# Kernel tuning notes

Hardware: AMD Instinct MI355X
Metric: run time of the kernel (lower is better)

## Reference

```python
import jax, jax.numpy as jnp
from jax import lax
import numpy as np

RADIUS = 5
ITERATION = 10
IMG_SHAPE = (2048, 2048, 3)


def make_side_window_kernels(r):
    # 8 directional side-window box kernels, each (2r+1)x(2r+1), minus identity at center
    k = np.ones((2 * r + 1, 1), dtype=np.float64) / (2 * r + 1)
    k_L = k.copy()
    k_L[r + 1:] = 0
    k_L = k_L / np.sum(k_L)
    k_R = k_L[::-1, :]

    def get_kernel(a, b):
        # repeat(a, K, axis=1) * repeat(b.T, K, axis=0) == outer(a, b)
        ab = a @ b.T
        ab = ab.copy()
        ab[r, r] -= 1.0  # residual form: filter - identity
        return ab

    kernel = np.stack([
        get_kernel(k_L, k_L), get_kernel(k_L, k_R),
        get_kernel(k_R, k_L), get_kernel(k_R, k_R),
        get_kernel(k_L, k), get_kernel(k_R, k),
        get_kernel(k, k_L), get_kernel(k, k_R),
    ]).astype(np.float32)
    return kernel[:, np.newaxis, :, :]  # (8, 1, K, K) OIHW


def setup_inputs() -> dict:
    key = jax.random.key(0)
    img = jax.random.uniform(key, IMG_SHAPE, dtype=jnp.float32)
    kernel = jnp.asarray(make_side_window_kernels(RADIUS))
    return {"img": img, "kernel": kernel}


def reference(img, kernel):
    r = RADIUS
    # edge-pad once (numpy 'edge' == jnp 'edge')
    U0 = jnp.pad(img, ((r, r), (r, r), (0, 0)), mode="edge")  # (Hp, Wp, C)

    def step(U, _):
        x = jnp.transpose(U, (2, 0, 1))[:, None]  # (C, 1, Hp, Wp)
        # cross-correlation with zero padding r (matches torch Conv2d padding=r)
        d = lax.conv_general_dilated(x, kernel, (1, 1), [(r, r), (r, r)])  # (C, 8, Hp, Wp)
        idx = jnp.argmin(jnp.abs(d), axis=1, keepdims=True)  # (C, 1, Hp, Wp)
        dm = jnp.take_along_axis(d, idx, axis=1)[:, 0]        # (C, Hp, Wp)
        return U + jnp.transpose(dm, (1, 2, 0)), None

    U, _ = lax.scan(step, U0, None, length=ITERATION)
    return U[r:-r, r:-r, :]
```

## Files before the change

kernel.cpp:

```cpp
#include <hip/hip_runtime.h>

#define H 2048
#define W 2048
#define C 3
#define RAD 5
#define P (H + 2*RAD)
#define RS 2064
#define PLANE ((size_t)P * RS)
#define NITER 10

#define BX 64
#define BY 16
#define EX (BX + 2*RAD)
#define EY (BY + 2*RAD)
#define LSTR (EX + 1)

__global__ void pad_kernel(const float* __restrict__ img, float* __restrict__ dst, int c) {
    int idx = blockIdx.x * blockDim.x + threadIdx.x;
    int total = P * P;
    if (idx >= total) return;
    int y = idx / P;
    int x = idx - y * P;
    int ys = min(max(y - RAD, 0), H - 1);
    int xs = min(max(x - RAD, 0), W - 1);
    dst[(size_t)y * RS + x] = img[((size_t)ys * W + xs) * C + c];
}

__global__ __launch_bounds__(256)
void step_kernel(const float* __restrict__ src, float* __restrict__ dst,
                 const float* __restrict__ kern) {
    __shared__ float sU[EY][LSTR];

    const float w36 = kern[0];
    const float c36 = kern[5 * 11 + 5];
    const float w66 = kern[4 * 121];
    const float c66 = kern[4 * 121 + 5 * 11 + 5];

    const int x0 = blockIdx.x * BX;
    const int y0 = blockIdx.y * BY;
    const int tid = threadIdx.y * 64 + threadIdx.x;

    for (int i = tid; i < EY * EX; i += 256) {
        int r   = i / EX;
        int col = i - r * EX;
        int gy = y0 - RAD + r;
        int gx = x0 - RAD + col;
        float v = 0.0f;
        if (gy >= 0 && gy < P && gx >= 0 && gx < P)
            v = src[(size_t)gy * RS + gx];
        sU[r][col] = v;
    }
    __syncthreads();

    const int tx = threadIdx.x;
    const int gx = x0 + tx;
    const bool xok = (gx < P);

    #pragma unroll 1
    for (int rr = threadIdx.y; rr < BY; rr += 4) {
        int gy = y0 + rr;
        if (!xok || gy >= P) continue;

        float a0 = 0.f, a1 = 0.f, a2 = 0.f, a3 = 0.f;
        float a4 = 0.f, a5 = 0.f, a6 = 0.f, a7 = 0.f;

        #pragma unroll
        for (int ky = 0; ky < 11; ++ky) {
            #pragma unroll
            for (int kx = 0; kx < 11; ++kx) {
                const float uv = sU[rr + ky][tx + kx];
                const bool Lv = (ky <= 5), Rv = (ky >= 5);
                const bool Lh = (kx <= 5), Rh = (kx >= 5);
                const bool ctr = (ky == 5) && (kx == 5);
                const float wc = ctr ? c36 : w36;
                const float ws = ctr ? c66 : w66;
                if (Lv && Lh) a0 = __fadd_rn(a0, __fmul_rn(wc, uv));
                if (Lv && Rh) a1 = __fadd_rn(a1, __fmul_rn(wc, uv));
                if (Rv && Lh) a2 = __fadd_rn(a2, __fmul_rn(wc, uv));
                if (Rv && Rh) a3 = __fadd_rn(a3, __fmul_rn(wc, uv));
                if (Lv)       a4 = __fadd_rn(a4, __fmul_rn(ws, uv));
                if (Rv)       a5 = __fadd_rn(a5, __fmul_rn(ws, uv));
                if (Lh)       a6 = __fadd_rn(a6, __fmul_rn(ws, uv));
                if (Rh)       a7 = __fadd_rn(a7, __fmul_rn(ws, uv));
            }
        }

        float best = a0, ba = fabsf(a0);
        float t;
        t = fabsf(a1); if (t < ba) { ba = t; best = a1; }
        t = fabsf(a2); if (t < ba) { ba = t; best = a2; }
        t = fabsf(a3); if (t < ba) { ba = t; best = a3; }
        t = fabsf(a4); if (t < ba) { ba = t; best = a4; }
        t = fabsf(a5); if (t < ba) { ba = t; best = a5; }
        t = fabsf(a6); if (t < ba) { ba = t; best = a6; }
        t = fabsf(a7); if (t < ba) { ba = t; best = a7; }

        const float u = sU[rr + RAD][tx + RAD];
        dst[(size_t)gy * RS + gx] = __fadd_rn(u, best);
    }
}

__global__ void crop_kernel(const float* __restrict__ src, float* __restrict__ dst, int c) {
    int idx = blockIdx.x * blockDim.x + threadIdx.x;
    int total = H * W;
    if (idx >= total) return;
    int y = idx / W;
    int x = idx - y * W;
    dst[((size_t)y * W + x) * C + c] = src[(size_t)(y + RAD) * RS + (x + RAD)];
}

extern "C" void kernel_launch(void* const* d_in, const int* in_sizes, int n_in,
                              void* d_out, int out_size, void* d_ws, size_t ws_size,
                              hipStream_t stream) {
    const float* img  = (const float*)d_in[0];
    const float* kern = (const float*)d_in[1];
    float* out = (float*)d_out;

    float* b0 = (float*)d_ws;
    float* b1 = b0 + PLANE;

    dim3 sgrid((P + BX - 1) / BX, (P + BY - 1) / BY, 1);
    dim3 sblock(64, 4, 1);

    for (int c = 0; c < C; ++c) {
        {
            int total = P * P;
            pad_kernel<<<(total + 255) / 256, 256, 0, stream>>>(img, b0, c);
        }
        for (int i = 0; i < NITER; ++i) {
            const float* s = (i & 1) ? b1 : b0;
            float*       d = (i & 1) ? b0 : b1;
            step_kernel<<<sgrid, sblock, 0, stream>>>(s, d, kern);
        }
        {
            int total = H * W;
            crop_kernel<<<(total + 255) / 256, 256, 0, stream>>>(b0, out, c);
        }
    }
}
```

Baseline: 1.915 ms.

## Compute four rows per thread with shared loads and batch channels via grid z

Each thread now computes four consecutive output rows, sweeping 14 shared-memory rows once and reusing each loaded value and its two weight products across up to four row accumulators. This cuts LDS reads and multiplies. Separately, when the workspace is large enough, all three channels run in one launch per iteration via blockIdx.z, cutting launch count and filling the GPU better. The cost is more accumulator registers (32 floats per thread), which may lower occupancy or cause spills.

```diff
diff --git a/kernel.cpp b/kernel.cpp
--- a/kernel.cpp
+++ b/kernel.cpp
@@ -15,15 +15,17 @@
 #define EY (BY + 2*RAD)
 #define LSTR (EX + 1)
 
-__global__ void pad_kernel(const float* __restrict__ img, float* __restrict__ dst, int c) {
+__global__ void pad_kernel(const float* __restrict__ img, float* __restrict__ dst, int c0) {
     int idx = blockIdx.x * blockDim.x + threadIdx.x;
     int total = P * P;
     if (idx >= total) return;
+    int c = c0 + blockIdx.z;
+    float* d = dst + (size_t)blockIdx.z * PLANE;
     int y = idx / P;
     int x = idx - y * P;
     int ys = min(max(y - RAD, 0), H - 1);
     int xs = min(max(x - RAD, 0), W - 1);
-    dst[(size_t)y * RS + x] = img[((size_t)ys * W + xs) * C + c];
+    d[(size_t)y * RS + x] = img[((size_t)ys * W + xs) * C + c];
 }
 
 __global__ __launch_bounds__(256)
@@ -38,6 +40,8 @@
 
     const int x0 = blockIdx.x * BX;
     const int y0 = blockIdx.y * BY;
+    const float* sp = src + (size_t)blockIdx.z * PLANE;
+    float*       dp = dst + (size_t)blockIdx.z * PLANE;
     const int tid = threadIdx.y * 64 + threadIdx.x;
 
     for (int i = tid; i < EY * EX; i += 256) {
@@ -47,46 +51,57 @@
         int gx = x0 - RAD + col;
         float v = 0.0f;
         if (gy >= 0 && gy < P && gx >= 0 && gx < P)
-            v = src[(size_t)gy * RS + gx];
+            v = sp[(size_t)gy * RS + gx];
         sU[r][col] = v;
     }
     __syncthreads();
 
     const int tx = threadIdx.x;
     const int gx = x0 + tx;
-    const bool xok = (gx < P);
+    const int r0 = threadIdx.y * 4;
 
-    #pragma unroll 1
-    for (int rr = threadIdx.y; rr < BY; rr += 4) {
-        int gy = y0 + rr;
-        if (!xok || gy >= P) continue;
+    float acc[4][8];
+    #pragma unroll
+    for (int rp = 0; rp < 4; ++rp)
+        #pragma unroll
+        for (int j = 0; j < 8; ++j)
+            acc[rp][j] = 0.0f;
 
-        float a0 = 0.f, a1 = 0.f, a2 = 0.f, a3 = 0.f;
-        float a4 = 0.f, a5 = 0.f, a6 = 0.f, a7 = 0.f;
-
+    #pragma unroll
+    for (int gr = 0; gr < 14; ++gr) {
         #pragma unroll
-        for (int ky = 0; ky < 11; ++ky) {
+        for (int kx = 0; kx < 11; ++kx) {
+            const float uv  = sU[r0 + gr][tx + kx];
+            const float p36 = __fmul_rn(w36, uv);
+            const float p66 = __fmul_rn(w66, uv);
             #pragma unroll
-            for (int kx = 0; kx < 11; ++kx) {
-                const float uv = sU[rr + ky][tx + kx];
+            for (int rp = 0; rp < 4; ++rp) {
+                const int ky = gr - rp;
+                if (ky < 0 || ky > 10) continue;
                 const bool Lv = (ky <= 5), Rv = (ky >= 5);
                 const bool Lh = (kx <= 5), Rh = (kx >= 5);
                 const bool ctr = (ky == 5) && (kx == 5);
-                const float wc = ctr ? c36 : w36;
-                const float ws = ctr ? c66 : w66;
-                if (Lv && Lh) a0 = __fadd_rn(a0, __fmul_rn(wc, uv));
-                if (Lv && Rh) a1 = __fadd_rn(a1, __fmul_rn(wc, uv));
-                if (Rv && Lh) a2 = __fadd_rn(a2, __fmul_rn(wc, uv));
-                if (Rv && Rh) a3 = __fadd_rn(a3, __fmul_rn(wc, uv));
-                if (Lv)       a4 = __fadd_rn(a4, __fmul_rn(ws, uv));
-                if (Rv)       a5 = __fadd_rn(a5, __fmul_rn(ws, uv));
-                if (Lh)       a6 = __fadd_rn(a6, __fmul_rn(ws, uv));
-                if (Rh)       a7 = __fadd_rn(a7, __fmul_rn(ws, uv));
+                const float pc = ctr ? __fmul_rn(c36, uv) : p36;
+                const float ps = ctr ? __fmul_rn(c66, uv) : p66;
+                if (Lv && Lh) acc[rp][0] = __fadd_rn(acc[rp][0], pc);
+                if (Lv && Rh) acc[rp][1] = __fadd_rn(acc[rp][1], pc);
+                if (Rv && Lh) acc[rp][2] = __fadd_rn(acc[rp][2], pc);
+                if (Rv && Rh) acc[rp][3] = __fadd_rn(acc[rp][3], pc);
+                if (Lv)       acc[rp][4] = __fadd_rn(acc[rp][4], ps);
+                if (Rv)       acc[rp][5] = __fadd_rn(acc[rp][5], ps);
+                if (Lh)       acc[rp][6] = __fadd_rn(acc[rp][6], ps);
+                if (Rh)       acc[rp][7] = __fadd_rn(acc[rp][7], ps);
             }
         }
+    }
 
-        float best = a0, ba = fabsf(a0);
-        float t;
+    #pragma unroll
+    for (int rp = 0; rp < 4; ++rp) {
+        const int gy = y0 + r0 + rp;
+        if (gx >= P || gy >= P) continue;
+        const float a0 = acc[rp][0], a1 = acc[rp][1], a2 = acc[rp][2], a3 = acc[rp][3];
+        const float a4 = acc[rp][4], a5 = acc[rp][5], a6 = acc[rp][6], a7 = acc[rp][7];
+        float best = a0, ba = fabsf(a0), t;
         t = fabsf(a1); if (t < ba) { ba = t; best = a1; }
         t = fabsf(a2); if (t < ba) { ba = t; best = a2; }
         t = fabsf(a3); if (t < ba) { ba = t; best = a3; }
@@ -94,19 +109,20 @@
         t = fabsf(a5); if (t < ba) { ba = t; best = a5; }
         t = fabsf(a6); if (t < ba) { ba = t; best = a6; }
         t = fabsf(a7); if (t < ba) { ba = t; best = a7; }
-
-        const float u = sU[rr + RAD][tx + RAD];
-        dst[(size_t)gy * RS + gx] = __fadd_rn(u, best);
+        const float u = sU[r0 + rp + RAD][tx + RAD];
+        dp[(size_t)gy * RS + gx] = __fadd_rn(u, best);
     }
 }
 
-__global__ void crop_kernel(const float* __restrict__ src, float* __restrict__ dst, int c) {
+__global__ void crop_kernel(const float* __restrict__ src, float* __restrict__ dst, int c0) {
     int idx = blockIdx.x * blockDim.x + threadIdx.x;
     int total = H * W;
     if (idx >= total) return;
+    int c = c0 + blockIdx.z;
+    const float* s = src + (size_t)blockIdx.z * PLANE;
     int y = idx / W;
     int x = idx - y * W;
-    dst[((size_t)y * W + x) * C + c] = src[(size_t)(y + RAD) * RS + (x + RAD)];
+    dst[((size_t)y * W + x) * C + c] = s[(size_t)(y + RAD) * RS + (x + RAD)];
 }
 
 extern "C" void kernel_launch(void* const* d_in, const int* in_sizes, int n_in,
@@ -116,25 +132,33 @@
     const float* kern = (const float*)d_in[1];
     float* out = (float*)d_out;
 
-    float* b0 = (float*)d_ws;
-    float* b1 = b0 + PLANE;
+    dim3 sblock(64, 4, 1);
+    const int gxb = (P + BX - 1) / BX;
+    const int gyb = (P + BY - 1) / BY;
+    const int padg = (P * P + 255) / 256;
+    const int crpg = (H * W + 255) / 256;
 
-    dim3 sgrid((P + BX - 1) / BX, (P + BY - 1) / BY, 1);
-    dim3 sblock(64, 4, 1);
-
-    for (int c = 0; c < C; ++c) {
-        {
-            int total = P * P;
-            pad_kernel<<<(total + 255) / 256, 256, 0, stream>>>(img, b0, c);
-        }
+    if (ws_size >= (size_t)6 * PLANE * sizeof(float)) {
+        float* b0 = (float*)d_ws;
+        float* b1 = b0 + 3 * PLANE;
+        pad_kernel<<<dim3(padg, 1, C), 256, 0, stream>>>(img, b0, 0);
         for (int i = 0; i < NITER; ++i) {
             const float* s = (i & 1) ? b1 : b0;
             float*       d = (i & 1) ? b0 : b1;
-            step_kernel<<<sgrid, sblock, 0, stream>>>(s, d, kern);
+            step_kernel<<<dim3(gxb, gyb, C), sblock, 0, stream>>>(s, d, kern);
         }
-        {
-            int total = H * W;
-            crop_kernel<<<(total + 255) / 256, 256, 0, stream>>>(b0, out, c);
+        crop_kernel<<<dim3(crpg, 1, C), 256, 0, stream>>>(b0, out, 0);
+    } else {
+        float* b0 = (float*)d_ws;
+        float* b1 = b0 + PLANE;
+        for (int c = 0; c < C; ++c) {
+            pad_kernel<<<dim3(padg, 1, 1), 256, 0, stream>>>(img, b0, c);
+            for (int i = 0; i < NITER; ++i) {
+                const float* s = (i & 1) ? b1 : b0;
+                float*       d = (i & 1) ? b0 : b1;
+                step_kernel<<<dim3(gxb, gyb, 1), sblock, 0, stream>>>(s, d, kern);
+            }
+            crop_kernel<<<dim3(crpg, 1, 1), 256, 0, stream>>>(b0, out, c);
         }
     }
 }
```

After: 3.956 ms. +106.6%, slower.
